# Kernel tuning notes

Measured on AMD Instinct MI355X. Metric: run time of the kernel, lower is better.

Reference implementation:

```python
import jax, jax.numpy as jnp
import numpy as np

B = 131072
NJ = 24
# SMPL parent tree (root at 0); PARENTS[j] is parent of joint j.
PARENTS = np.array([-1, 0, 0, 0, 1, 2, 3, 4, 5, 6, 7, 8, 9, 9, 9, 12, 13, 14, 16, 17, 18, 19, 20, 21], dtype=np.int32)
PARENT_IDS = PARENTS[1:]  # parents of joints 1..NJ-1 (all < child index)


def setup_inputs() -> dict:
    key = jax.random.key(0)
    k1, k2, k3 = jax.random.split(key, 3)
    theta = jax.random.normal(k1, (B, NJ, 3), dtype=jnp.float32) * 0.2
    rest_pose = jax.random.normal(k2, (NJ, 3), dtype=jnp.float32)
    bone_factor = jax.random.uniform(k3, (1, NJ - 1, 1, 1), dtype=jnp.float32, minval=0.5, maxval=1.5)
    parents = jnp.asarray(PARENT_IDS)
    return {"theta": theta, "rest_pose": rest_pose, "bone_factor": bone_factor, "parents": parents}


def axisang_to_rot(v):
    """Rodrigues: (M,3) axis-angle -> (M,3,3) rotation matrices."""
    eps = 1e-12
    angle = jnp.sqrt(jnp.sum(v * v, axis=-1, keepdims=True) + eps)  # (M,1)
    ax = v / angle
    c = jnp.cos(angle)[..., None]  # (M,1,1)
    s = jnp.sin(angle)[..., None]
    x, y, z = ax[:, 0], ax[:, 1], ax[:, 2]
    zero = jnp.zeros_like(x)
    K = jnp.stack([zero, -z, y, z, zero, -x, -y, x, zero], axis=-1).reshape(-1, 3, 3)
    outer = ax[:, :, None] * ax[:, None, :]
    I = jnp.eye(3, dtype=v.dtype)
    return c * I + (1.0 - c) * outer + s * K


def reference(theta, rest_pose, bone_factor, parents):
    Bd, NJd, _ = theta.shape
    rots = axisang_to_rot(theta.reshape(-1, 3)).reshape(Bd, NJd, 3, 3)
    rp = jnp.broadcast_to(rest_pose[None], (Bd, NJd, 3))
    # root local-to-world: [R_root | t_root] padded to 4x4
    root34 = jnp.concatenate([rots[:, 0], rp[:, 0, :, None]], axis=-1)  # (B,3,4)
    bottom = jnp.broadcast_to(jnp.array([0.0, 0.0, 0.0, 1.0], theta.dtype)[None, None], (Bd, 1, 4))
    root_l2w = jnp.concatenate([root34, bottom], axis=1)  # (B,4,4)
    # children relative transforms: [R_child | bone_vector]
    children_rots = rots[:, 1:]                              # (B,NJ-1,3,3)
    bv = (rp[:, 1:] - rp[:, parents])[..., None]             # (B,NJ-1,3,1)
    bf = jnp.sqrt(bone_factor ** 2 + 1e-36)                  # force positive, as in torch code
    bv = bv * bf
    rel = jnp.concatenate([children_rots, bv], axis=-1)      # (B,NJ-1,3,4)
    bottom2 = jnp.broadcast_to(jnp.array([0.0, 0.0, 0.0, 1.0], theta.dtype)[None, None, None], (Bd, NJd - 1, 1, 4))
    rel = jnp.concatenate([rel, bottom2], axis=-2)           # (B,NJ-1,4,4)
    # sequential kinematic chain: compose with static parent indices
    l2ws = [root_l2w]
    for i in range(NJd - 1):
        p = int(PARENT_IDS[i])
        l2ws.append(l2ws[p] @ rel[:, i])
    l2ws = jnp.stack(l2ws, axis=1)  # (B,NJ,4,4)
    kp3d = l2ws[..., :3, -1]
    orient = l2ws[..., :3, :3]
    return kp3d, orient, l2ws
```

## Files before the change

### kernel.cpp

```cpp
#include <hip/hip_runtime.h>
#include <math.h>

#define NJ   24
#define TPB  256
#define IPB  32
#define ST   73

static constexpr int PAR[NJ] = {-1,0,0,0,1,2,3,4,5,6,7,8,9,9,9,12,13,14,16,17,18,19,20,21};

__global__ __launch_bounds__(TPB, 4) void fk_kernel(
    const float* __restrict__ theta,
    const float* __restrict__ rest_pose,
    const float* __restrict__ bone_factor,
    float* __restrict__ kp3d,
    float* __restrict__ orient,
    float* __restrict__ l2ws,
    int Bn)
{
    __shared__ float4 ls[IPB * ST];

    const int tid   = threadIdx.x;
    const int item0 = blockIdx.x * IPB;
    if (item0 >= Bn) return;

    const int it  = tid / 3;
    const int row = tid % 3;
    const int gi  = item0 + it;
    if (tid < 96 && gi < Bn) {
        const float4* th4 = reinterpret_cast<const float4*>(theta) + (size_t)gi * 18;
        float4 tv[18];
        #pragma unroll
        for (int i = 0; i < 18; ++i) tv[i] = th4[i];

        float4 rows_[NJ];
        #pragma unroll
        for (int sub = 0; sub < 3; ++sub) {
            float t[24];
            #pragma unroll
            for (int i = 0; i < 6; ++i) {
                const float4 v = tv[sub * 6 + i];
                t[i*4+0] = v.x; t[i*4+1] = v.y; t[i*4+2] = v.z; t[i*4+3] = v.w;
            }
            #pragma unroll
            for (int jj = 0; jj < 8; ++jj) {
                const int j = sub * 8 + jj;
                const float x = t[jj*3+0], y = t[jj*3+1], z = t[jj*3+2];
                const float ang = sqrtf(x*x + y*y + z*z + 1e-12f);
                const float inv = 1.0f / ang;
                const float ux = x*inv, uy = y*inv, uz = z*inv;
                const float s  = __sinf(ang);
                const float cs = __cosf(ang);
                const float ic = 1.0f - cs;
                const float xy = ic*ux*uy, xz = ic*ux*uz, yz = ic*uy*uz;
                const float sx = s*ux, sy = s*uy, sz = s*uz;
                const float R00 = cs + ic*ux*ux, R01 = xy - sz, R02 = xz + sy;
                const float R10 = xy + sz, R11 = cs + ic*uy*uy, R12 = yz - sx;
                const float R20 = xz - sy, R21 = yz + sx, R22 = cs + ic*uz*uz;

                float4 p; float bx, by, bz;
                if (j == 0) {
                    p  = make_float4(row == 0 ? 1.f : 0.f,
                                     row == 1 ? 1.f : 0.f,
                                     row == 2 ? 1.f : 0.f, 0.f);
                    bx = rest_pose[0]; by = rest_pose[1]; bz = rest_pose[2];
                } else {
                    p = rows_[PAR[j]];
                    float bf = bone_factor[j - 1];
                    bf = sqrtf(bf*bf + 1e-36f);
                    bx = (rest_pose[j*3+0] - rest_pose[PAR[j]*3+0]) * bf;
                    by = (rest_pose[j*3+1] - rest_pose[PAR[j]*3+1]) * bf;
                    bz = (rest_pose[j*3+2] - rest_pose[PAR[j]*3+2]) * bf;
                }
                float4 nr;
                nr.x = p.x*R00 + p.y*R10 + p.z*R20;
                nr.y = p.x*R01 + p.y*R11 + p.z*R21;
                nr.z = p.x*R02 + p.y*R12 + p.z*R22;
                nr.w = p.x*bx  + p.y*by  + p.z*bz + p.w;
                rows_[j] = nr;
                ls[it * ST + j * 3 + row] = nr;
            }
        }
    }
    __syncthreads();

    const float* lf = reinterpret_cast<const float*>(ls);
    const int n_i = min(IPB, Bn - item0);

    {
        float4* dst = reinterpret_cast<float4*>(l2ws) + (size_t)item0 * 96;
        #pragma unroll
        for (int k = 0; k < 12; ++k) {
            const int q  = k * TPB + tid;
            const int i  = q / 96, off = q % 96;
            const int jj = off >> 2, rr = off & 3;
            float4 v;
            if (rr == 3) v = make_float4(0.f, 0.f, 0.f, 1.f);
            else         v = ls[i * ST + jj * 3 + rr];
            if (i < n_i) dst[q] = v;
        }
    }
    {
        float4* dst = reinterpret_cast<float4*>(orient) + (size_t)item0 * 54;
        #pragma unroll
        for (int k = 0; k < 7; ++k) {
            const int q = k * TPB + tid;
            if (k < 6 || q < 1728) {
                float v[4];
                #pragma unroll
                for (int m = 0; m < 4; ++m) {
                    const int f  = q * 4 + m;
                    const int i  = f / 216, r2 = f % 216;
                    const int jj = r2 / 9,  mm = r2 % 9;
                    v[m] = lf[(i * ST + jj * 3 + mm / 3) * 4 + mm % 3];
                }
                if (q / 54 < n_i) dst[q] = make_float4(v[0], v[1], v[2], v[3]);
            }
        }
    }
    {
        float4* dst = reinterpret_cast<float4*>(kp3d) + (size_t)item0 * 18;
        #pragma unroll
        for (int k = 0; k < 3; ++k) {
            const int q = k * TPB + tid;
            if (k < 2 || q < 576) {
                float v[4];
                #pragma unroll
                for (int m = 0; m < 4; ++m) {
                    const int f  = q * 4 + m;
                    const int i  = f / 72, r2 = f % 72;
                    const int jj = r2 / 3, rw = r2 % 3;
                    v[m] = lf[(i * ST + jj * 3 + rw) * 4 + 3];
                }
                if (q / 18 < n_i) dst[q] = make_float4(v[0], v[1], v[2], v[3]);
            }
        }
    }
}

extern "C" void kernel_launch(void* const* d_in, const int* in_sizes, int n_in,
                              void* d_out, int out_size, void* d_ws, size_t ws_size,
                              hipStream_t stream) {
    const float* theta       = (const float*)d_in[0];
    const float* rest_pose   = (const float*)d_in[1];
    const float* bone_factor = (const float*)d_in[2];

    const int Bn = in_sizes[0] / (NJ * 3);
    const size_t BNJ = (size_t)Bn * NJ;

    float* out    = (float*)d_out;
    float* kp3d   = out;
    float* orient = out + BNJ * 3;
    float* l2ws   = out + BNJ * 12;

    const int grid = (Bn + IPB - 1) / IPB;
    fk_kernel<<<grid, TPB, 0, stream>>>(theta, rest_pose, bone_factor,
                                        kp3d, orient, l2ws, Bn);
}
```

Baseline: 86.77 us.

## Use persistent blocks with double-buffered shared tiles overlapping compute and stores

Replaces one-block-per-32-items with a fixed grid of persistent blocks. Each block loops over 16-item tiles and double-buffers shared memory, computing the next tile while the current one is written out. The aim is to overlap the serial kinematic-chain compute, done by only 48 threads, with the global stores. The cost is that compute now uses an even smaller fraction of threads per tile, and the fixed grid reduces how many blocks are in flight at once.

```diff
diff --git a/kernel.cpp b/kernel.cpp
--- a/kernel.cpp
+++ b/kernel.cpp
@@ -3,108 +3,107 @@
 
 #define NJ   24
 #define TPB  256
-#define IPB  32
+#define IPT  16
 #define ST   73
+#define NBLK 1024
 
 static constexpr int PAR[NJ] = {-1,0,0,0,1,2,3,4,5,6,7,8,9,9,9,12,13,14,16,17,18,19,20,21};
 
-__global__ __launch_bounds__(TPB, 4) void fk_kernel(
+__device__ __forceinline__ void compute_tile(
+    int tile, int Bn, int tid,
     const float* __restrict__ theta,
     const float* __restrict__ rest_pose,
     const float* __restrict__ bone_factor,
-    float* __restrict__ kp3d,
-    float* __restrict__ orient,
-    float* __restrict__ l2ws,
-    int Bn)
+    float4* __restrict__ bf4)
 {
-    __shared__ float4 ls[IPB * ST];
-
-    const int tid   = threadIdx.x;
-    const int item0 = blockIdx.x * IPB;
-    if (item0 >= Bn) return;
-
     const int it  = tid / 3;
     const int row = tid % 3;
-    const int gi  = item0 + it;
-    if (tid < 96 && gi < Bn) {
-        const float4* th4 = reinterpret_cast<const float4*>(theta) + (size_t)gi * 18;
-        float4 tv[18];
+    const int gi  = tile * IPT + it;
+    if (tid >= 48 || gi >= Bn) return;
+
+    const float4* th4 = reinterpret_cast<const float4*>(theta) + (size_t)gi * 18;
+    float4 tv[18];
+    #pragma unroll
+    for (int i = 0; i < 18; ++i) tv[i] = th4[i];
+
+    float4 rows_[NJ];
+    #pragma unroll
+    for (int sub = 0; sub < 3; ++sub) {
+        float t[24];
         #pragma unroll
-        for (int i = 0; i < 18; ++i) tv[i] = th4[i];
+        for (int i = 0; i < 6; ++i) {
+            const float4 v = tv[sub * 6 + i];
+            t[i*4+0] = v.x; t[i*4+1] = v.y; t[i*4+2] = v.z; t[i*4+3] = v.w;
+        }
+        #pragma unroll
+        for (int jj = 0; jj < 8; ++jj) {
+            const int j = sub * 8 + jj;
+            const float x = t[jj*3+0], y = t[jj*3+1], z = t[jj*3+2];
+            const float ang = sqrtf(x*x + y*y + z*z + 1e-12f);
+            const float inv = 1.0f / ang;
+            const float ux = x*inv, uy = y*inv, uz = z*inv;
+            const float s  = __sinf(ang);
+            const float cs = __cosf(ang);
+            const float ic = 1.0f - cs;
+            const float xy = ic*ux*uy, xz = ic*ux*uz, yz = ic*uy*uz;
+            const float sx = s*ux, sy = s*uy, sz = s*uz;
+            const float R00 = cs + ic*ux*ux, R01 = xy - sz, R02 = xz + sy;
+            const float R10 = xy + sz, R11 = cs + ic*uy*uy, R12 = yz - sx;
+            const float R20 = xz - sy, R21 = yz + sx, R22 = cs + ic*uz*uz;
 
-        float4 rows_[NJ];
-        #pragma unroll
-        for (int sub = 0; sub < 3; ++sub) {
-            float t[24];
-            #pragma unroll
-            for (int i = 0; i < 6; ++i) {
-                const float4 v = tv[sub * 6 + i];
-                t[i*4+0] = v.x; t[i*4+1] = v.y; t[i*4+2] = v.z; t[i*4+3] = v.w;
+            float4 p; float bx, by, bz;
+            if (j == 0) {
+                p  = make_float4(row == 0 ? 1.f : 0.f,
+                                 row == 1 ? 1.f : 0.f,
+                                 row == 2 ? 1.f : 0.f, 0.f);
+                bx = rest_pose[0]; by = rest_pose[1]; bz = rest_pose[2];
+            } else {
+                p = rows_[PAR[j]];
+                float bfv = bone_factor[j - 1];
+                bfv = sqrtf(bfv*bfv + 1e-36f);
+                bx = (rest_pose[j*3+0] - rest_pose[PAR[j]*3+0]) * bfv;
+                by = (rest_pose[j*3+1] - rest_pose[PAR[j]*3+1]) * bfv;
+                bz = (rest_pose[j*3+2] - rest_pose[PAR[j]*3+2]) * bfv;
             }
-            #pragma unroll
-            for (int jj = 0; jj < 8; ++jj) {
-                const int j = sub * 8 + jj;
-                const float x = t[jj*3+0], y = t[jj*3+1], z = t[jj*3+2];
-                const float ang = sqrtf(x*x + y*y + z*z + 1e-12f);
-                const float inv = 1.0f / ang;
-                const float ux = x*inv, uy = y*inv, uz = z*inv;
-                const float s  = __sinf(ang);
-                const float cs = __cosf(ang);
-                const float ic = 1.0f - cs;
-                const float xy = ic*ux*uy, xz = ic*ux*uz, yz = ic*uy*uz;
-                const float sx = s*ux, sy = s*uy, sz = s*uz;
-                const float R00 = cs + ic*ux*ux, R01 = xy - sz, R02 = xz + sy;
-                const float R10 = xy + sz, R11 = cs + ic*uy*uy, R12 = yz - sx;
-                const float R20 = xz - sy, R21 = yz + sx, R22 = cs + ic*uz*uz;
-
-                float4 p; float bx, by, bz;
-                if (j == 0) {
-                    p  = make_float4(row == 0 ? 1.f : 0.f,
-                                     row == 1 ? 1.f : 0.f,
-                                     row == 2 ? 1.f : 0.f, 0.f);
-                    bx = rest_pose[0]; by = rest_pose[1]; bz = rest_pose[2];
-                } else {
-                    p = rows_[PAR[j]];
-                    float bf = bone_factor[j - 1];
-                    bf = sqrtf(bf*bf + 1e-36f);
-                    bx = (rest_pose[j*3+0] - rest_pose[PAR[j]*3+0]) * bf;
-                    by = (rest_pose[j*3+1] - rest_pose[PAR[j]*3+1]) * bf;
-                    bz = (rest_pose[j*3+2] - rest_pose[PAR[j]*3+2]) * bf;
-                }
-                float4 nr;
-                nr.x = p.x*R00 + p.y*R10 + p.z*R20;
-                nr.y = p.x*R01 + p.y*R11 + p.z*R21;
-                nr.z = p.x*R02 + p.y*R12 + p.z*R22;
-                nr.w = p.x*bx  + p.y*by  + p.z*bz + p.w;
-                rows_[j] = nr;
-                ls[it * ST + j * 3 + row] = nr;
-            }
+            float4 nr;
+            nr.x = p.x*R00 + p.y*R10 + p.z*R20;
+            nr.y = p.x*R01 + p.y*R11 + p.z*R21;
+            nr.z = p.x*R02 + p.y*R12 + p.z*R22;
+            nr.w = p.x*bx  + p.y*by  + p.z*bz + p.w;
+            rows_[j] = nr;
+            bf4[it * ST + j * 3 + row] = nr;
         }
     }
-    __syncthreads();
+}
 
-    const float* lf = reinterpret_cast<const float*>(ls);
-    const int n_i = min(IPB, Bn - item0);
+__device__ __forceinline__ void flush_tile(
+    int tile, int Bn, int tid,
+    const float4* __restrict__ bf4,
+    float4* __restrict__ l2g, float4* __restrict__ org, float4* __restrict__ kpg)
+{
+    const float* lf = reinterpret_cast<const float*>(bf4);
+    const int gbase = tile * IPT;
+    const int n_i = min(IPT, Bn - gbase);
 
     {
-        float4* dst = reinterpret_cast<float4*>(l2ws) + (size_t)item0 * 96;
+        float4* dst = l2g + (size_t)gbase * 96;
         #pragma unroll
-        for (int k = 0; k < 12; ++k) {
+        for (int k = 0; k < 6; ++k) {
             const int q  = k * TPB + tid;
             const int i  = q / 96, off = q % 96;
             const int jj = off >> 2, rr = off & 3;
             float4 v;
             if (rr == 3) v = make_float4(0.f, 0.f, 0.f, 1.f);
-            else         v = ls[i * ST + jj * 3 + rr];
+            else         v = bf4[i * ST + jj * 3 + rr];
             if (i < n_i) dst[q] = v;
         }
     }
     {
-        float4* dst = reinterpret_cast<float4*>(orient) + (size_t)item0 * 54;
+        float4* dst = org + (size_t)gbase * 54;
         #pragma unroll
-        for (int k = 0; k < 7; ++k) {
+        for (int k = 0; k < 4; ++k) {
             const int q = k * TPB + tid;
-            if (k < 6 || q < 1728) {
+            if (k < 3 || q < 864) {
                 float v[4];
                 #pragma unroll
                 for (int m = 0; m < 4; ++m) {
@@ -118,11 +117,11 @@
         }
     }
     {
-        float4* dst = reinterpret_cast<float4*>(kp3d) + (size_t)item0 * 18;
+        float4* dst = kpg + (size_t)gbase * 18;
         #pragma unroll
-        for (int k = 0; k < 3; ++k) {
+        for (int k = 0; k < 2; ++k) {
             const int q = k * TPB + tid;
-            if (k < 2 || q < 576) {
+            if (k < 1 || q < 288) {
                 float v[4];
                 #pragma unroll
                 for (int m = 0; m < 4; ++m) {
@@ -134,6 +133,40 @@
                 if (q / 18 < n_i) dst[q] = make_float4(v[0], v[1], v[2], v[3]);
             }
         }
+    }
+}
+
+__global__ __launch_bounds__(TPB, 4) void fk_kernel(
+    const float* __restrict__ theta,
+    const float* __restrict__ rest_pose,
+    const float* __restrict__ bone_factor,
+    float* __restrict__ kp3d,
+    float* __restrict__ orient,
+    float* __restrict__ l2ws,
+    int Bn)
+{
+    __shared__ float4 buf[2][IPT * ST];
+
+    const int tid   = threadIdx.x;
+    const int tiles = (Bn + IPT - 1) / IPT;
+    const int t0    = (tiles + gridDim.x - 1) / gridDim.x;
+    const int start = blockIdx.x * t0;
+    const int end   = min(start + t0, tiles);
+    if (start >= end) return;
+
+    float4* l2g = reinterpret_cast<float4*>(l2ws);
+    float4* org = reinterpret_cast<float4*>(orient);
+    float4* kpg = reinterpret_cast<float4*>(kp3d);
+
+    compute_tile(start, Bn, tid, theta, rest_pose, bone_factor, buf[0]);
+    __syncthreads();
+
+    for (int i = start; i < end; ++i) {
+        const int d = (i - start) & 1;
+        flush_tile(i, Bn, tid, buf[d], l2g, org, kpg);
+        if (i + 1 < end)
+            compute_tile(i + 1, Bn, tid, theta, rest_pose, bone_factor, buf[d ^ 1]);
+        __syncthreads();
     }
 }
 
@@ -152,7 +185,8 @@
     float* orient = out + BNJ * 3;
     float* l2ws   = out + BNJ * 12;
 
-    const int grid = (Bn + IPB - 1) / IPB;
+    const int tiles = (Bn + IPT - 1) / IPT;
+    const int grid  = min(NBLK, tiles);
     fk_kernel<<<grid, TPB, 0, stream>>>(theta, rest_pose, bone_factor,
                                         kp3d, orient, l2ws, Bn);
 }
```

Result: slower. 123.8 us (+42.7%).
